# Optimization experiments

Measured on AMD Instinct MI355X. Metric: run time of the kernel, lower is better.

The kernel has to match this reference:

```python
import jax, jax.numpy as jnp
import numpy as np
import math

EMBED_DIM = 768
NUM_HEADS = 12
HEAD_DIM = EMBED_DIM // NUM_HEADS
R = 16
LORA_ALPHA = 16
SCALING = LORA_ALPHA / math.sqrt(R)  # 4.0
U = 1.0  # ramp_up_steps=0 -> u()=1.0


def lora_linear(x, W, b, A):
    # base F.linear + SingLoRA delta: delta_W = A @ A.T (symmetric)
    base = x @ W.T + b
    delta_W = A @ A.T  # [D, D]
    return base + (x @ delta_W.T) * (U * SCALING)


def setup_inputs() -> dict:
    key = jax.random.key(0)
    ks = jax.random.split(key, 16)
    B, S, D = 2, 2048, EMBED_DIM
    inv = 1.0 / math.sqrt(D)
    d = {
        'query': jax.random.normal(ks[0], (B, S, D), jnp.float32),
        'key': jax.random.normal(ks[1], (B, S, D), jnp.float32),
        'value': jax.random.normal(ks[2], (B, S, D), jnp.float32),
        'Wq': jax.random.normal(ks[3], (D, D), jnp.float32) * inv,
        'bq': jax.random.normal(ks[4], (D,), jnp.float32) * 0.01,
        'Aq': jax.random.normal(ks[5], (D, R), jnp.float32) * 0.01,
        'Wk': jax.random.normal(ks[6], (D, D), jnp.float32) * inv,
        'bk': jax.random.normal(ks[7], (D,), jnp.float32) * 0.01,
        'Ak': jax.random.normal(ks[8], (D, R), jnp.float32) * 0.01,
        'Wv': jax.random.normal(ks[9], (D, D), jnp.float32) * inv,
        'bv': jax.random.normal(ks[10], (D,), jnp.float32) * 0.01,
        'Av': jax.random.normal(ks[11], (D, R), jnp.float32) * 0.01,
        'Wo': jax.random.normal(ks[12], (D, D), jnp.float32) * inv,
        'bo': jax.random.normal(ks[13], (D,), jnp.float32) * 0.01,
    }
    return d


def reference(query, key, value, Wq, bq, Aq, Wk, bk, Ak, Wv, bv, Av, Wo, bo):
    B, S, D = query.shape
    H, hd = NUM_HEADS, HEAD_DIM
    q = lora_linear(query, Wq, bq, Aq)
    k = lora_linear(key, Wk, bk, Ak)
    v = lora_linear(value, Wv, bv, Av)
    # [B, S, D] -> [B, H, S, hd]
    q = q.reshape(B, S, H, hd).transpose(0, 2, 1, 3)
    k = k.reshape(B, S, H, hd).transpose(0, 2, 1, 3)
    v = v.reshape(B, S, H, hd).transpose(0, 2, 1, 3)
    scores = jnp.einsum('bhqd,bhkd->bhqk', q, k) / math.sqrt(hd)
    attn = jax.nn.softmax(scores, axis=-1)
    out = jnp.einsum('bhqk,bhkd->bhqd', attn, v)  # [B, H, S, hd]
    out = out.transpose(0, 2, 1, 3).reshape(B, S, D)
    out = out @ Wo.T + bo
    return out
```

## Files before the change

kernel.cpp:

```cpp
#include <hip/hip_runtime.h>
#include <math.h>
#include <stdint.h>

#define D 768
#define S 2048
#define B_ 2
#define NROWS 4096
#define H 12
#define HD 64
#define R_ 16

typedef _Float16 half_t;
typedef _Float16 half8 __attribute__((ext_vector_type(8)));
typedef _Float16 half4 __attribute__((ext_vector_type(4)));
typedef float floatx4 __attribute__((ext_vector_type(4)));

#define MFMA32(a, b, c) __builtin_amdgcn_mfma_f32_16x16x32_f16(a, b, c, 0, 0, 0)
#define MFMA16(a, b, c) __builtin_amdgcn_mfma_f32_16x16x16f16(a, b, c, 0, 0, 0)
#define EXP2F(x) __builtin_amdgcn_exp2f(x)

__device__ __forceinline__ void gl_lds16(const void* gp, half_t* lp) {
  __builtin_amdgcn_global_load_lds(
      (const __attribute__((address_space(1))) void*)(gp),
      (__attribute__((address_space(3))) void*)(lp), 16, 0, 0);
}

__global__ __launch_bounds__(256) void prep_kernel(
    const float* __restrict__ q, const float* __restrict__ k,
    const float* __restrict__ v, half_t* __restrict__ xq,
    half_t* __restrict__ xk, half_t* __restrict__ xv,
    const float* __restrict__ Wq, const float* __restrict__ Aq,
    const float* __restrict__ Wk, const float* __restrict__ Ak,
    const float* __restrict__ Wv, const float* __restrict__ Av,
    const float* __restrict__ Wo, half_t* __restrict__ Mq,
    half_t* __restrict__ Mk, half_t* __restrict__ Mv,
    half_t* __restrict__ Mo) {
  const int bid = blockIdx.x;
  if (bid < 9216) {
    const int y = bid / 3072;
    const float* x = (y == 0) ? q : (y == 1) ? k : v;
    half_t* o = (y == 0) ? xq : (y == 1) ? xk : xv;
    int i = (bid - y * 3072) * 1024 + threadIdx.x * 4;
    float4 vv = *reinterpret_cast<const float4*>(x + i);
    half_t tmp[4] = {(half_t)vv.x, (half_t)vv.y, (half_t)vv.z, (half_t)vv.w};
    *reinterpret_cast<uint64_t*>(o + i) = *reinterpret_cast<uint64_t*>(tmp);
  } else {
    const int u = bid - 9216;
    const int y = u / 2304;
    const float* W = (y == 0) ? Wq : (y == 1) ? Wk : (y == 2) ? Wv : Wo;
    const float* A = (y == 0) ? Aq : (y == 1) ? Ak : (y == 2) ? Av : nullptr;
    half_t* M = (y == 0) ? Mq : (y == 1) ? Mk : (y == 2) ? Mv : Mo;
    int idx = (u - y * 2304) * 256 + threadIdx.x;
    int j = idx / D;
    int kk = idx - j * D;
    float acc = W[idx];
    if (A != nullptr) {
      float s = 0.f;
#pragma unroll
      for (int r = 0; r < R_; ++r) s += A[kk * R_ + r] * A[j * R_ + r];
      acc += 4.0f * s;
    }
    M[idx] = (half_t)acc;
  }
}

__global__ __launch_bounds__(256) void gemm_qkv_kernel(
    const half_t* __restrict__ x0, const half_t* __restrict__ x1,
    const half_t* __restrict__ x2, const half_t* __restrict__ m0,
    const half_t* __restrict__ m1, const half_t* __restrict__ m2,
    const float* __restrict__ b0, const float* __restrict__ b1,
    const float* __restrict__ b2, half_t* __restrict__ o0,
    half_t* __restrict__ o1, half_t* __restrict__ o2) {
  constexpr int AG = 8;
  constexpr int G = AG + 16;
  constexpr int PB = G * 512;
  constexpr int TRS = 72;
  __shared__ __align__(16) half_t smem[2 * PB];

  const int z = blockIdx.z;
  const half_t* X = (z == 0) ? x0 : (z == 1) ? x1 : x2;
  const half_t* M = (z == 0) ? m0 : (z == 1) ? m1 : m2;
  const float* bias = (z == 0) ? b0 : (z == 1) ? b1 : b2;
  half_t* Out = (z == 0) ? o0 : (z == 1) ? o1 : o2;

  const int tid = threadIdx.x;
  const int lane = tid & 63;
  const int wv = tid >> 6;
  const int lr = lane & 15;
  const int lq = lane >> 4;
  const int row0 = blockIdx.y * 64;
  const int j0 = blockIdx.x * 128;
  const int wc = wv;

  floatx4 acc[4][2] = {};

#define GSTAGE(bufi, k0)                                                       \
  do {                                                                         \
    _Pragma("unroll") for (int gi = 0; gi < 6; ++gi) {                         \
      int g = wv * 6 + gi;                                                     \
      if (g < AG) {                                                            \
        int t = g >> 1, c = g & 1;                                             \
        gl_lds16(                                                              \
            X + (size_t)(row0 + t * 16 + lr) * D + (k0) + c * 32 + lq * 8,     \
            smem + (bufi)*PB + g * 512);                                       \
      } else {                                                                 \
        int g2 = g - AG;                                                       \
        int u = g2 >> 1, c = g2 & 1;                                           \
        gl_lds16(                                                              \
            M + (size_t)(j0 + u * 16 + lr) * D + (k0) + c * 32 + lq * 8,       \
            smem + (bufi)*PB + AG * 512 + g2 * 512);                           \
      }                                                                        \
    }                                                                          \
  } while (0)

  GSTAGE(0, 0);
  __syncthreads();

  for (int it = 0; it < D / 64; ++it) {
    const int cur = it & 1;
    if (it + 1 < D / 64) GSTAGE(cur ^ 1, (it + 1) * 64);
    const half_t* Ab = smem + cur * PB;
    const half_t* Bb = Ab + AG * 512;
#pragma unroll
    for (int c = 0; c < 2; ++c) {
      half8 af[4], bf[2];
#pragma unroll
      for (int t = 0; t < 4; ++t)
        af[t] = *reinterpret_cast<const half8*>(
            &Ab[((t * 2 + c) * 64 + lane) * 8]);
#pragma unroll
      for (int u = 0; u < 2; ++u)
        bf[u] = *reinterpret_cast<const half8*>(
            &Bb[(((wc * 2 + u) * 2 + c) * 64 + lane) * 8]);
#pragma unroll
      for (int t = 0; t < 4; ++t)
#pragma unroll
        for (int u = 0; u < 2; ++u) acc[t][u] = MFMA32(af[t], bf[u], acc[t][u]);
    }
    __syncthreads();
  }
#undef GSTAGE

  float bv[2];
#pragma unroll
  for (int u = 0; u < 2; ++u) bv[u] = bias[j0 + (wc * 2 + u) * 16 + lr];

  if (z == 2) {
#pragma unroll
    for (int t = 0; t < 4; ++t) {
#pragma unroll
      for (int u = 0; u < 2; ++u) {
        int c_local = (wc * 2 + u) * 16 + lr;
#pragma unroll
        for (int r = 0; r < 4; ++r) {
          int r_local = t * 16 + lq * 4 + r;
          smem[c_local * TRS + r_local] = (half_t)(acc[t][u][r] + bv[u]);
        }
      }
    }
    __syncthreads();
    const int bb = row0 >> 11;
    const int s_base = row0 & 2047;
#pragma unroll
    for (int it = 0; it < 4; ++it) {
      int unit = it * 256 + tid;
      int c_local = unit >> 3;
      int chunk = unit & 7;
      half8 vv =
          *reinterpret_cast<const half8*>(&smem[c_local * TRS + chunk * 8]);
      int gc = j0 + c_local;
      int hh = gc >> 6, dd = gc & 63;
      *reinterpret_cast<half8*>(
          &Out[((size_t)(bb * H + hh) * HD + dd) * S + s_base + chunk * 8]) = vv;
    }
    return;
  }

#pragma unroll
  for (int t = 0; t < 4; ++t) {
#pragma unroll
    for (int u = 0; u < 2; ++u) {
#pragma unroll
      for (int r = 0; r < 4; ++r) {
        int gr = row0 + t * 16 + lq * 4 + r;
        int gc = j0 + (wc * 2 + u) * 16 + lr;
        Out[(size_t)gr * D + gc] = (half_t)(acc[t][u][r] + bv[u]);
      }
    }
  }
}

__global__ __launch_bounds__(256) void gemm_o_kernel(
    const half_t* __restrict__ Xh, const half_t* __restrict__ M,
    const float* __restrict__ bias, float* __restrict__ Out) {
  constexpr int AG = 8;
  constexpr int G = AG + 16;
  constexpr int PB = G * 512;
  __shared__ __align__(16) half_t smem[2 * PB];

  const int tid = threadIdx.x;
  const int lane = tid & 63;
  const int wv = tid >> 6;
  const int lr = lane & 15;
  const int lq = lane >> 4;
  const int row0 = blockIdx.y * 64;
  const int j0 = blockIdx.x * 128;
  const int wc = wv;

  floatx4 acc[4][2] = {};

#define GSTAGE(bufi, k0)                                                       \
  do {                                                                         \
    _Pragma("unroll") for (int gi = 0; gi < 6; ++gi) {                         \
      int g = wv * 6 + gi;                                                     \
      if (g < AG) {                                                            \
        int t = g >> 1, c = g & 1;                                             \
        gl_lds16(                                                              \
            Xh + (size_t)(row0 + t * 16 + lr) * D + (k0) + c * 32 + lq * 8,    \
            smem + (bufi)*PB + g * 512);                                       \
      } else {                                                                 \
        int g2 = g - AG;                                                       \
        int u = g2 >> 1, c = g2 & 1;                                           \
        gl_lds16(                                                              \
            M + (size_t)(j0 + u * 16 + lr) * D + (k0) + c * 32 + lq * 8,       \
            smem + (bufi)*PB + AG * 512 + g2 * 512);                           \
      }                                                                        \
    }                                                                          \
  } while (0)

  GSTAGE(0, 0);
  __syncthreads();

  for (int it = 0; it < D / 64; ++it) {
    const int cur = it & 1;
    if (it + 1 < D / 64) GSTAGE(cur ^ 1, (it + 1) * 64);
    const half_t* Ab = smem + cur * PB;
    const half_t* Bb = Ab + AG * 512;
#pragma unroll
    for (int c = 0; c < 2; ++c) {
      half8 af[4], bf[2];
#pragma unroll
      for (int t = 0; t < 4; ++t)
        af[t] = *reinterpret_cast<const half8*>(
            &Ab[((t * 2 + c) * 64 + lane) * 8]);
#pragma unroll
      for (int u = 0; u < 2; ++u)
        bf[u] = *reinterpret_cast<const half8*>(
            &Bb[(((wc * 2 + u) * 2 + c) * 64 + lane) * 8]);
#pragma unroll
      for (int t = 0; t < 4; ++t)
#pragma unroll
        for (int u = 0; u < 2; ++u) acc[t][u] = MFMA32(af[t], bf[u], acc[t][u]);
    }
    __syncthreads();
  }
#undef GSTAGE

  float bv[2];
#pragma unroll
  for (int u = 0; u < 2; ++u) bv[u] = bias[j0 + (wc * 2 + u) * 16 + lr];
#pragma unroll
  for (int t = 0; t < 4; ++t) {
#pragma unroll
    for (int u = 0; u < 2; ++u) {
#pragma unroll
      for (int r = 0; r < 4; ++r) {
        int gr = row0 + t * 16 + lq * 4 + r;
        int gc = j0 + (wc * 2 + u) * 16 + lr;
        Out[(size_t)gr * D + gc] = acc[t][u][r] + bv[u];
      }
    }
  }
}

__global__ __launch_bounds__(512, 6) void attn_mfma_kernel(
    const half_t* __restrict__ Qh, const half_t* __restrict__ Kh,
    const half_t* __restrict__ Vt_g, half_t* __restrict__ Oh) {
  __shared__ __align__(16) half_t smem[16384];
  half_t* Ks = smem;
  half_t* Vs = smem + 8192;

  const int tid = threadIdx.x;
  const int lane = tid & 63;
  const int wv = tid >> 6;
  const int t_ = wv & 3;
  const int half_ = wv >> 2;
  const int lr = lane & 15;
  const int lq = lane >> 4;
  const int q0 = blockIdx.x * 64;
  const int h = blockIdx.y;
  const int b = blockIdx.z;
  const size_t base = (size_t)b * S * D + h * HD;
  const size_t vtbase = (size_t)(b * H + h) * HD * (size_t)S;
  const int qw = q0 + t_ * 16;

  const half_t qscale = (half_t)0.18033688f;
  half8 qf[2];
#pragma unroll
  for (int c = 0; c < 2; ++c) {
    half8 qv = *reinterpret_cast<const half8*>(
        &Qh[base + (size_t)(qw + lr) * D + c * 32 + lq * 8]);
#pragma unroll
    for (int j = 0; j < 8; ++j) qv[j] = qv[j] * qscale;
    qf[c] = qv;
  }

  half4 ones;
#pragma unroll
  for (int j = 0; j < 4; ++j) ones[j] = (half_t)1.0f;

  floatx4 o[4] = {};
  floatx4 ol = {};

#define STAGE(bufi, kb)                                                        \
  do {                                                                         \
    _Pragma("unroll") for (int gi = 0; gi < 2; ++gi) {                         \
      int g = wv * 2 + gi;                                                     \
      if (g < 8) {                                                             \
        int u = g >> 1, c = g & 1;                                             \
        gl_lds16(                                                              \
            Kh + base + (size_t)((kb) + u * 16 + lr) * D + c * 32 + lq * 8,    \
            Ks + (bufi)*4096 + g * 512);                                       \
      } else {                                                                 \
        int gv = g - 8;                                                        \
        int ud = gv >> 1, c = gv & 1;                                          \
        gl_lds16(                                                              \
            Vt_g + vtbase + (size_t)(ud * 16 + lr) * S + (kb) + c * 32 +       \
                lq * 8,                                                        \
            Vs + (bufi)*4096 + gv * 512);                                      \
      }                                                                        \
    }                                                                          \
  } while (0)

  STAGE(0, 0);
  __syncthreads();

  for (int it = 0; it < S / 64; ++it) {
    const int cur = it & 1;
    if (it + 1 < S / 64) STAGE(cur ^ 1, (it + 1) * 64);

#pragma unroll
    for (int ui = 0; ui < 2; ++ui) {
      const int u = half_ * 2 + ui;
      half8 kf0 = *reinterpret_cast<const half8*>(
          &Ks[cur * 4096 + ((u * 2 + 0) * 64 + lane) * 8]);
      half8 kf1 = *reinterpret_cast<const half8*>(
          &Ks[cur * 4096 + ((u * 2 + 1) * 64 + lane) * 8]);
      floatx4 st = {};
      st = MFMA32(kf0, qf[0], st);
      st = MFMA32(kf1, qf[1], st);
      half4 pf;
      pf[0] = (half_t)EXP2F(st[0]);
      pf[1] = (half_t)EXP2F(st[1]);
      pf[2] = (half_t)EXP2F(st[2]);
      pf[3] = (half_t)EXP2F(st[3]);
#pragma unroll
      for (int ud = 0; ud < 4; ++ud) {
        half4 vf = *reinterpret_cast<const half4*>(
            &Vs[cur * 4096 + ((ud * 2 + (u >> 1)) * 64 +
                              ((((u & 1) * 2) + (lq >> 1)) * 16 + lr)) *
                                 8 +
                (lq & 1) * 4]);
        o[ud] = MFMA16(pf, vf, o[ud]);
      }
      ol = MFMA16(pf, ones, ol);
    }
    __syncthreads();
  }
#undef STAGE

  float* red = (float*)smem;
  const int slot = t_ * 64 + lane;
  if (half_ == 1) {
#pragma unroll
    for (int comp = 0; comp < 16; ++comp)
      red[comp * 260 + slot] = o[comp >> 2][comp & 3];
#pragma unroll
    for (int r = 0; r < 4; ++r) red[(16 + r) * 260 + slot] = ol[r];
  }
  __syncthreads();
  if (half_ == 0) {
#pragma unroll
    for (int comp = 0; comp < 16; ++comp)
      o[comp >> 2][comp & 3] += red[comp * 260 + slot];
    float linv[4];
#pragma unroll
    for (int r = 0; r < 4; ++r)
      linv[r] = 1.0f / (ol[r] + red[(16 + r) * 260 + slot]);
#pragma unroll
    for (int ud = 0; ud < 4; ++ud) {
#pragma unroll
      for (int r = 0; r < 4; ++r) {
        int row = qw + lq * 4 + r;
        int col = h * HD + ud * 16 + lr;
        Oh[(size_t)(b * S + row) * D + col] = (half_t)(o[ud][r] * linv[r]);
      }
    }
  }
}

extern "C" void kernel_launch(void* const* d_in, const int* in_sizes, int n_in,
                              void* d_out, int out_size, void* d_ws,
                              size_t ws_size, hipStream_t stream) {
  const float* query = (const float*)d_in[0];
  const float* key   = (const float*)d_in[1];
  const float* value = (const float*)d_in[2];
  const float* Wq = (const float*)d_in[3];
  const float* bq = (const float*)d_in[4];
  const float* Aq = (const float*)d_in[5];
  const float* Wk = (const float*)d_in[6];
  const float* bk = (const float*)d_in[7];
  const float* Ak = (const float*)d_in[8];
  const float* Wv = (const float*)d_in[9];
  const float* bv = (const float*)d_in[10];
  const float* Av = (const float*)d_in[11];
  const float* Wo = (const float*)d_in[12];
  const float* bo = (const float*)d_in[13];
  float* out = (float*)d_out;

  half_t* hw = (half_t*)d_ws;
  const size_t XSZ = (size_t)NROWS * D;
  const size_t MSZ = (size_t)D * D;
  half_t* xq = hw;
  half_t* xk = xq + XSZ;
  half_t* xv = xk + XSZ;
  half_t* qh = xv + XSZ;
  half_t* kh = qh + XSZ;
  half_t* vt = kh + XSZ;
  half_t* ab = vt + XSZ;
  half_t* Mq = ab + XSZ;
  half_t* Mk = Mq + MSZ;
  half_t* Mv = Mk + MSZ;
  half_t* Mo = Mv + MSZ;

  prep_kernel<<<18432, 256, 0, stream>>>(query, key, value, xq, xk, xv, Wq, Aq,
                                         Wk, Ak, Wv, Av, Wo, Mq, Mk, Mv, Mo);

  dim3 gq(D / 128, NROWS / 64, 3);
  gemm_qkv_kernel<<<gq, 256, 0, stream>>>(xq, xk, xv, Mq, Mk, Mv, bq, bk, bv,
                                          qh, kh, vt);

  dim3 ga(S / 64, H, B_);
  attn_mfma_kernel<<<ga, 512, 0, stream>>>(qh, kh, vt, ab);

  dim3 go(D / 128, NROWS / 64, 1);
  gemm_o_kernel<<<go, 256, 0, stream>>>(ab, Mo, bo, out);
}
```

Baseline: 233.0 us.

## Load per-wave B/K operands directly into registers and halve O-projection tile width

Result: slower. 349.6 us (+50.0%).

```diff
diff --git a/kernel.cpp b/kernel.cpp
--- a/kernel.cpp
+++ b/kernel.cpp
@@ -71,11 +71,8 @@
     const float* __restrict__ b0, const float* __restrict__ b1,
     const float* __restrict__ b2, half_t* __restrict__ o0,
     half_t* __restrict__ o1, half_t* __restrict__ o2) {
-  constexpr int AG = 8;
-  constexpr int G = AG + 16;
-  constexpr int PB = G * 512;
   constexpr int TRS = 72;
-  __shared__ __align__(16) half_t smem[2 * PB];
+  __shared__ __align__(16) half_t smem[9216];
 
   const int z = blockIdx.z;
   const half_t* X = (z == 0) ? x0 : (z == 1) ? x1 : x2;
@@ -93,53 +90,60 @@
   const int wc = wv;
 
   floatx4 acc[4][2] = {};
-
-#define GSTAGE(bufi, k0)                                                       \
-  do {                                                                         \
-    _Pragma("unroll") for (int gi = 0; gi < 6; ++gi) {                         \
-      int g = wv * 6 + gi;                                                     \
-      if (g < AG) {                                                            \
-        int t = g >> 1, c = g & 1;                                             \
-        gl_lds16(                                                              \
-            X + (size_t)(row0 + t * 16 + lr) * D + (k0) + c * 32 + lq * 8,     \
-            smem + (bufi)*PB + g * 512);                                       \
-      } else {                                                                 \
-        int g2 = g - AG;                                                       \
-        int u = g2 >> 1, c = g2 & 1;                                           \
-        gl_lds16(                                                              \
-            M + (size_t)(j0 + u * 16 + lr) * D + (k0) + c * 32 + lq * 8,       \
-            smem + (bufi)*PB + AG * 512 + g2 * 512);                           \
-      }                                                                        \
+  half8 bA[2][2], bB[2][2];
+
+#define STAGEA(bufi, k0)                                                       \
+  do {                                                                         \
+    _Pragma("unroll") for (int gi = 0; gi < 2; ++gi) {                         \
+      int g = wv * 2 + gi;                                                     \
+      int t = g >> 1, c = g & 1;                                               \
+      gl_lds16(X + (size_t)(row0 + t * 16 + lr) * D + (k0) + c * 32 + lq * 8,  \
+               smem + (bufi)*4096 + g * 512);                                  \
     }                                                                          \
   } while (0)
 
-  GSTAGE(0, 0);
+#define LOADB(BF, k0)                                                          \
+  do {                                                                         \
+    _Pragma("unroll") for (int u = 0; u < 2; ++u)                              \
+        _Pragma("unroll") for (int c = 0; c < 2; ++c) BF[u][c] =               \
+        *reinterpret_cast<const half8*>(                                       \
+            &M[(size_t)(j0 + (wc * 2 + u) * 16 + lr) * D + (k0) + c * 32 +     \
+               lq * 8]);                                                       \
+  } while (0)
+
+#define COMPUTEG(BF, bufi)                                                     \
+  do {                                                                         \
+    _Pragma("unroll") for (int c = 0; c < 2; ++c) {                            \
+      half8 af[4];                                                             \
+      _Pragma("unroll") for (int t = 0; t < 4; ++t) af[t] =                    \
+          *reinterpret_cast<const half8*>(                                     \
+              &smem[(bufi)*4096 + ((t * 2 + c) * 64 + lane) * 8]);             \
+      _Pragma("unroll") for (int t = 0; t < 4; ++t)                            \
+          _Pragma("unroll") for (int u = 0; u < 2; ++u) acc[t][u] =            \
+          MFMA32(af[t], BF[u][c], acc[t][u]);                                  \
+    }                                                                          \
+  } while (0)
+
+  STAGEA(0, 0);
+  LOADB(bA, 0);
   __syncthreads();
 
-  for (int it = 0; it < D / 64; ++it) {
-    const int cur = it & 1;
-    if (it + 1 < D / 64) GSTAGE(cur ^ 1, (it + 1) * 64);
-    const half_t* Ab = smem + cur * PB;
-    const half_t* Bb = Ab + AG * 512;
-#pragma unroll
-    for (int c = 0; c < 2; ++c) {
-      half8 af[4], bf[2];
-#pragma unroll
-      for (int t = 0; t < 4; ++t)
-        af[t] = *reinterpret_cast<const half8*>(
-            &Ab[((t * 2 + c) * 64 + lane) * 8]);
-#pragma unroll
-      for (int u = 0; u < 2; ++u)
-        bf[u] = *reinterpret_cast<const half8*>(
-            &Bb[(((wc * 2 + u) * 2 + c) * 64 + lane) * 8]);
-#pragma unroll
-      for (int t = 0; t < 4; ++t)
-#pragma unroll
-        for (int u = 0; u < 2; ++u) acc[t][u] = MFMA32(af[t], bf[u], acc[t][u]);
-    }
-    __syncthreads();
-  }
-#undef GSTAGE
+#pragma unroll 1
+  for (int it = 0; it < D / 64; it += 2) {
+    STAGEA(1, (it + 1) * 64);
+    LOADB(bB, (it + 1) * 64);
+    COMPUTEG(bA, 0);
+    __syncthreads();
+    if (it + 2 < D / 64) {
+      STAGEA(0, (it + 2) * 64);
+      LOADB(bA, (it + 2) * 64);
+    }
+    COMPUTEG(bB, 1);
+    __syncthreads();
+  }
+#undef STAGEA
+#undef LOADB
+#undef COMPUTEG
 
   float bv[2];
 #pragma unroll
@@ -193,10 +197,7 @@
 __global__ __launch_bounds__(256) void gemm_o_kernel(
     const half_t* __restrict__ Xh, const half_t* __restrict__ M,
     const float* __restrict__ bias, float* __restrict__ Out) {
-  constexpr int AG = 8;
-  constexpr int G = AG + 16;
-  constexpr int PB = G * 512;
-  __shared__ __align__(16) half_t smem[2 * PB];
+  __shared__ __align__(16) half_t smem[8192];
 
   const int tid = threadIdx.x;
   const int lane = tid & 63;
@@ -204,71 +205,70 @@
   const int lr = lane & 15;
   const int lq = lane >> 4;
   const int row0 = blockIdx.y * 64;
-  const int j0 = blockIdx.x * 128;
+  const int j0 = blockIdx.x * 64;
   const int wc = wv;
 
-  floatx4 acc[4][2] = {};
-
-#define GSTAGE(bufi, k0)                                                       \
-  do {                                                                         \
-    _Pragma("unroll") for (int gi = 0; gi < 6; ++gi) {                         \
-      int g = wv * 6 + gi;                                                     \
-      if (g < AG) {                                                            \
-        int t = g >> 1, c = g & 1;                                             \
-        gl_lds16(                                                              \
-            Xh + (size_t)(row0 + t * 16 + lr) * D + (k0) + c * 32 + lq * 8,    \
-            smem + (bufi)*PB + g * 512);                                       \
-      } else {                                                                 \
-        int g2 = g - AG;                                                       \
-        int u = g2 >> 1, c = g2 & 1;                                           \
-        gl_lds16(                                                              \
-            M + (size_t)(j0 + u * 16 + lr) * D + (k0) + c * 32 + lq * 8,       \
-            smem + (bufi)*PB + AG * 512 + g2 * 512);                           \
-      }                                                                        \
+  floatx4 acc[4] = {};
+  half8 bA[2], bB[2];
+
+#define STAGEA(bufi, k0)                                                       \
+  do {                                                                         \
+    _Pragma("unroll") for (int gi = 0; gi < 2; ++gi) {                         \
+      int g = wv * 2 + gi;                                                     \
+      int t = g >> 1, c = g & 1;                                               \
+      gl_lds16(Xh + (size_t)(row0 + t * 16 + lr) * D + (k0) + c * 32 + lq * 8, \
+               smem + (bufi)*4096 + g * 512);                                  \
     }                                                                          \
   } while (0)
 
-  GSTAGE(0, 0);
+#define LOADB(BF, k0)                                                          \
+  do {                                                                         \
+    _Pragma("unroll") for (int c = 0; c < 2; ++c) BF[c] =                      \
+        *reinterpret_cast<const half8*>(                                       \
+            &M[(size_t)(j0 + wc * 16 + lr) * D + (k0) + c * 32 + lq * 8]);     \
+  } while (0)
+
+#define COMPUTEG(BF, bufi)                                                     \
+  do {                                                                         \
+    _Pragma("unroll") for (int c = 0; c < 2; ++c) {                            \
+      half8 af[4];                                                             \
+      _Pragma("unroll") for (int t = 0; t < 4; ++t) af[t] =                    \
+          *reinterpret_cast<const half8*>(                                     \
+              &smem[(bufi)*4096 + ((t * 2 + c) * 64 + lane) * 8]);             \
+      _Pragma("unroll") for (int t = 0; t < 4; ++t) acc[t] =                   \
+          MFMA32(af[t], BF[c], acc[t]);                                        \
+    }                                                                          \
+  } while (0)
+
+  STAGEA(0, 0);
+  LOADB(bA, 0);
   __syncthreads();
 
-  for (int it = 0; it < D / 64; ++it) {
-    const int cur = it & 1;
-    if (it + 1 < D / 64) GSTAGE(cur ^ 1, (it + 1) * 64);
-    const half_t* Ab = smem + cur * PB;
-    const half_t* Bb = Ab + AG * 512;
-#pragma unroll
-    for (int c = 0; c < 2; ++c) {
-      half8 af[4], bf[2];
-#pragma unroll
-      for (int t = 0; t < 4; ++t)
-        af[t] = *reinterpret_cast<const half8*>(
-            &Ab[((t * 2 + c) * 64 + lane) * 8]);
-#pragma unroll
-      for (int u = 0; u < 2; ++u)
-        bf[u] = *reinterpret_cast<const half8*>(
-            &Bb[(((wc * 2 + u) * 2 + c) * 64 + lane) * 8]);
-#pragma unroll
-      for (int t = 0; t < 4; ++t)
-#pragma unroll
-        for (int u = 0; u < 2; ++u) acc[t][u] = MFMA32(af[t], bf[u], acc[t][u]);
-    }
-    __syncthreads();
-  }
-#undef GSTAGE
-
-  float bv[2];
-#pragma unroll
-  for (int u = 0; u < 2; ++u) bv[u] = bias[j0 + (wc * 2 + u) * 16 + lr];
+#pragma unroll 1
+  for (int it = 0; it < D / 64; it += 2) {
+    STAGEA(1, (it + 1) * 64);
+    LOADB(bB, (it + 1) * 64);
+    COMPUTEG(bA, 0);
+    __syncthreads();
+    if (it + 2 < D / 64) {
+      STAGEA(0, (it + 2) * 64);
+      LOADB(bA, (it + 2) * 64);
+    }
+    COMPUTEG(bB, 1);
+    __syncthreads();
+  }
+#undef STAGEA
+#undef LOADB
+#undef COMPUTEG
+
+  float bv = bias[j0 + wc * 16 + lr];
 #pragma unroll
   for (int t = 0; t < 4; ++t) {
 #pragma unroll
-    for (int u = 0; u < 2; ++u) {
-#pragma unroll
-      for (int r = 0; r < 4; ++r) {
-        int gr = row0 + t * 16 + lq * 4 + r;
-        int gc = j0 + (wc * 2 + u) * 16 + lr;
-        Out[(size_t)gr * D + gc] = acc[t][u][r] + bv[u];
-      }
+    for (int r = 0; r < 4; ++r) {
+      int gr = row0 + t * 16 + lq * 4 + r;
+      int gc = j0 + wc * 16 + lr;
+      Out[(size_t)gr * D + gc] = acc[t][r] + bv;
     }
   }
 }
@@ -276,9 +276,8 @@
 __global__ __launch_bounds__(512, 6) void attn_mfma_kernel(
     const half_t* __restrict__ Qh, const half_t* __restrict__ Kh,
     const half_t* __restrict__ Vt_g, half_t* __restrict__ Oh) {
-  __shared__ __align__(16) half_t smem[16384];
-  half_t* Ks = smem;
-  half_t* Vs = smem + 8192;
+  __shared__ __align__(16) half_t smem[12288];
+  half_t* Vs = smem;
 
   const int tid = threadIdx.x;
   const int lane = tid & 63;
@@ -311,63 +310,70 @@
 
   floatx4 o[4] = {};
   floatx4 ol = {};
-
-#define STAGE(bufi, kb)                                                        \
-  do {                                                                         \
-    _Pragma("unroll") for (int gi = 0; gi < 2; ++gi) {                         \
-      int g = wv * 2 + gi;                                                     \
-      if (g < 8) {                                                             \
-        int u = g >> 1, c = g & 1;                                             \
-        gl_lds16(                                                              \
-            Kh + base + (size_t)((kb) + u * 16 + lr) * D + c * 32 + lq * 8,    \
-            Ks + (bufi)*4096 + g * 512);                                       \
-      } else {                                                                 \
-        int gv = g - 8;                                                        \
-        int ud = gv >> 1, c = gv & 1;                                          \
-        gl_lds16(                                                              \
-            Vt_g + vtbase + (size_t)(ud * 16 + lr) * S + (kb) + c * 32 +       \
-                lq * 8,                                                        \
-            Vs + (bufi)*4096 + gv * 512);                                      \
+  half8 kf0[2][2], kf1[2][2];
+
+#define STAGEV(bufi, kb)                                                       \
+  do {                                                                         \
+    int ud = wv >> 1, c = wv & 1;                                              \
+    gl_lds16(                                                                  \
+        Vt_g + vtbase + (size_t)(ud * 16 + lr) * S + (kb) + c * 32 + lq * 8,   \
+        Vs + (bufi)*4096 + wv * 512);                                          \
+  } while (0)
+
+#define LOADK(KF, kb)                                                          \
+  do {                                                                         \
+    _Pragma("unroll") for (int ui = 0; ui < 2; ++ui)                           \
+        _Pragma("unroll") for (int c = 0; c < 2; ++c) KF[ui][c] =              \
+        *reinterpret_cast<const half8*>(                                       \
+            &Kh[base + (size_t)((kb) + (half_ * 2 + ui) * 16 + lr) * D +       \
+                c * 32 + lq * 8]);                                             \
+  } while (0)
+
+#define ACOMPUTE(KF, CUR)                                                      \
+  do {                                                                         \
+    _Pragma("unroll") for (int ui = 0; ui < 2; ++ui) {                         \
+      const int u = half_ * 2 + ui;                                            \
+      floatx4 st = {};                                                         \
+      st = MFMA32(KF[ui][0], qf[0], st);                                       \
+      st = MFMA32(KF[ui][1], qf[1], st);                                       \
+      half4 pf;                                                                \
+      pf[0] = (half_t)EXP2F(st[0]);                                            \
+      pf[1] = (half_t)EXP2F(st[1]);                                            \
+      pf[2] = (half_t)EXP2F(st[2]);                                            \
+      pf[3] = (half_t)EXP2F(st[3]);                                            \
+      _Pragma("unroll") for (int ud = 0; ud < 4; ++ud) {                       \
+        half4 vf = *reinterpret_cast<const half4*>(                            \
+            &Vs[(CUR)*4096 +                                                   \
+                ((ud * 2 + (u >> 1)) * 64 +                                    \
+                 ((((u & 1) * 2) + (lq >> 1)) * 16 + lr)) *                    \
+                    8 +                                                        \
+                (lq & 1) * 4]);                                                \
+        o[ud] = MFMA16(pf, vf, o[ud]);                                         \
       }                                                                        \
+      ol = MFMA16(pf, ones, ol);                                               \
     }                                                                          \
   } while (0)
 
-  STAGE(0, 0);
+  STAGEV(0, 0);
+  LOADK(kf0, 0);
   __syncthreads();
 
-  for (int it = 0; it < S / 64; ++it) {
-    const int cur = it & 1;
-    if (it + 1 < S / 64) STAGE(cur ^ 1, (it + 1) * 64);
-
-#pragma unroll
-    for (int ui = 0; ui < 2; ++ui) {
-      const int u = half_ * 2 + ui;
-      half8 kf0 = *reinterpret_cast<const half8*>(
-          &Ks[cur * 4096 + ((u * 2 + 0) * 64 + lane) * 8]);
-      half8 kf1 = *reinterpret_cast<const half8*>(
-          &Ks[cur * 4096 + ((u * 2 + 1) * 64 + lane) * 8]);
-      floatx4 st = {};
-      st = MFMA32(kf0, qf[0], st);
-      st = MFMA32(kf1, qf[1], st);
-      half4 pf;
-      pf[0] = (half_t)EXP2F(st[0]);
-      pf[1] = (half_t)EXP2F(st[1]);
-      pf[2] = (half_t)EXP2F(st[2]);
-      pf[3] = (half_t)EXP2F(st[3]);
-#pragma unroll
-      for (int ud = 0; ud < 4; ++ud) {
-        half4 vf = *reinterpret_cast<const half4*>(
-            &Vs[cur * 4096 + ((ud * 2 + (u >> 1)) * 64 +
-                              ((((u & 1) * 2) + (lq >> 1)) * 16 + lr)) *
-                                 8 +
-                (lq & 1) * 4]);
-        o[ud] = MFMA16(pf, vf, o[ud]);
-      }
-      ol = MFMA16(pf, ones, ol);
-    }
-    __syncthreads();
-  }
-#undef STAGE
+#pragma unroll 1
+  for (int it = 0; it < S / 64; it += 2) {
+    STAGEV(1, (it + 1) * 64);
+    LOADK(kf1, (it + 1) * 64);
+    ACOMPUTE(kf0, 0);
+    __syncthreads();
+    if (it + 2 < S / 64) {
+      STAGEV(0, (it + 2) * 64);
+      LOADK(kf0, (it + 2) * 64);
+    }
+    ACOMPUTE(kf1, 1);
+    __syncthreads();
+  }
+#undef STAGEV
+#undef LOADK
+#undef ACOMPUTE
 
   float* red = (float*)smem;
   const int slot = t_ * 64 + lane;
@@ -443,6 +449,6 @@
   dim3 ga(S / 64, H, B_);
   attn_mfma_kernel<<<ga, 512, 0, stream>>>(qh, kh, vt, ab);
 
-  dim3 go(D / 128, NROWS / 64, 1);
+  dim3 go(D / 64, NROWS / 64, 1);
   gemm_o_kernel<<<go, 256, 0, stream>>>(ab, Mo, bo, out);
 }
```

## Write V in MFMA-fragment layout and shrink output-projection GEMM tiles

Applied to the files above, without the earlier changes.

After: 223.1 us. -4.3%, faster.

```diff
diff --git a/kernel.cpp b/kernel.cpp
--- a/kernel.cpp
+++ b/kernel.cpp
@@ -24,6 +24,7 @@
       (const __attribute__((address_space(1))) void*)(gp),
       (__attribute__((address_space(3))) void*)(lp), 16, 0, 0);
 }
+
 
 __global__ __launch_bounds__(256) void prep_kernel(
     const float* __restrict__ q, const float* __restrict__ k,
@@ -74,7 +75,6 @@
   constexpr int AG = 8;
   constexpr int G = AG + 16;
   constexpr int PB = G * 512;
-  constexpr int TRS = 72;
   __shared__ __align__(16) half_t smem[2 * PB];
 
   const int z = blockIdx.z;
@@ -146,32 +146,22 @@
   for (int u = 0; u < 2; ++u) bv[u] = bias[j0 + (wc * 2 + u) * 16 + lr];
 
   if (z == 2) {
+    const int bb = row0 >> 11;
+    const int kb = (row0 & 2047) >> 6;
 #pragma unroll
     for (int t = 0; t < 4; ++t) {
 #pragma unroll
       for (int u = 0; u < 2; ++u) {
-        int c_local = (wc * 2 + u) * 16 + lr;
-#pragma unroll
-        for (int r = 0; r < 4; ++r) {
-          int r_local = t * 16 + lq * 4 + r;
-          smem[c_local * TRS + r_local] = (half_t)(acc[t][u][r] + bv[u]);
-        }
+        int gc = j0 + (wc * 2 + u) * 16 + lr;
+        int hh = gc >> 6;
+        int ud = (wc * 2 + u) & 3;
+        half4 hv;
+#pragma unroll
+        for (int r = 0; r < 4; ++r) hv[r] = (half_t)(acc[t][u][r] + bv[u]);
+        size_t addr = ((size_t)(bb * H + hh) * HD) * S + (size_t)kb * 4096 +
+                      (ud * 2 + (t >> 1)) * 512 + lane * 8 + (t & 1) * 4;
+        *reinterpret_cast<half4*>(&Out[addr]) = hv;
       }
-    }
-    __syncthreads();
-    const int bb = row0 >> 11;
-    const int s_base = row0 & 2047;
-#pragma unroll
-    for (int it = 0; it < 4; ++it) {
-      int unit = it * 256 + tid;
-      int c_local = unit >> 3;
-      int chunk = unit & 7;
-      half8 vv =
-          *reinterpret_cast<const half8*>(&smem[c_local * TRS + chunk * 8]);
-      int gc = j0 + c_local;
-      int hh = gc >> 6, dd = gc & 63;
-      *reinterpret_cast<half8*>(
-          &Out[((size_t)(bb * H + hh) * HD + dd) * S + s_base + chunk * 8]) = vv;
     }
     return;
   }
@@ -194,7 +184,7 @@
     const half_t* __restrict__ Xh, const half_t* __restrict__ M,
     const float* __restrict__ bias, float* __restrict__ Out) {
   constexpr int AG = 8;
-  constexpr int G = AG + 16;
+  constexpr int G = 16;
   constexpr int PB = G * 512;
   __shared__ __align__(16) half_t smem[2 * PB];
 
@@ -204,15 +194,16 @@
   const int lr = lane & 15;
   const int lq = lane >> 4;
   const int row0 = blockIdx.y * 64;
-  const int j0 = blockIdx.x * 128;
-  const int wc = wv;
-
-  floatx4 acc[4][2] = {};
+  const int j0 = blockIdx.x * 64;
+  const int wr = wv >> 1;
+  const int wc = wv & 1;
+
+  floatx4 acc[2][2] = {};
 
 #define GSTAGE(bufi, k0)                                                       \
   do {                                                                         \
-    _Pragma("unroll") for (int gi = 0; gi < 6; ++gi) {                         \
-      int g = wv * 6 + gi;                                                     \
+    _Pragma("unroll") for (int gi = 0; gi < 4; ++gi) {                         \
+      int g = wv * 4 + gi;                                                     \
       if (g < AG) {                                                            \
         int t = g >> 1, c = g & 1;                                             \
         gl_lds16(                                                              \
@@ -238,17 +229,17 @@
     const half_t* Bb = Ab + AG * 512;
 #pragma unroll
     for (int c = 0; c < 2; ++c) {
-      half8 af[4], bf[2];
-#pragma unroll
-      for (int t = 0; t < 4; ++t)
+      half8 af[2], bf[2];
+#pragma unroll
+      for (int t = 0; t < 2; ++t)
         af[t] = *reinterpret_cast<const half8*>(
-            &Ab[((t * 2 + c) * 64 + lane) * 8]);
+            &Ab[(((wr * 2 + t) * 2 + c) * 64 + lane) * 8]);
 #pragma unroll
       for (int u = 0; u < 2; ++u)
         bf[u] = *reinterpret_cast<const half8*>(
             &Bb[(((wc * 2 + u) * 2 + c) * 64 + lane) * 8]);
 #pragma unroll
-      for (int t = 0; t < 4; ++t)
+      for (int t = 0; t < 2; ++t)
 #pragma unroll
         for (int u = 0; u < 2; ++u) acc[t][u] = MFMA32(af[t], bf[u], acc[t][u]);
     }
@@ -260,12 +251,12 @@
 #pragma unroll
   for (int u = 0; u < 2; ++u) bv[u] = bias[j0 + (wc * 2 + u) * 16 + lr];
 #pragma unroll
-  for (int t = 0; t < 4; ++t) {
+  for (int t = 0; t < 2; ++t) {
 #pragma unroll
     for (int u = 0; u < 2; ++u) {
 #pragma unroll
       for (int r = 0; r < 4; ++r) {
-        int gr = row0 + t * 16 + lq * 4 + r;
+        int gr = row0 + (wr * 2 + t) * 16 + lq * 4 + r;
         int gc = j0 + (wc * 2 + u) * 16 + lr;
         Out[(size_t)gr * D + gc] = acc[t][u][r] + bv[u];
       }
@@ -275,7 +266,7 @@
 
 __global__ __launch_bounds__(512, 6) void attn_mfma_kernel(
     const half_t* __restrict__ Qh, const half_t* __restrict__ Kh,
-    const half_t* __restrict__ Vt_g, half_t* __restrict__ Oh) {
+    const half_t* __restrict__ Vt2, half_t* __restrict__ Oh) {
   __shared__ __align__(16) half_t smem[16384];
   half_t* Ks = smem;
   half_t* Vs = smem + 8192;
@@ -323,11 +314,8 @@
             Ks + (bufi)*4096 + g * 512);                                       \
       } else {                                                                 \
         int gv = g - 8;                                                        \
-        int ud = gv >> 1, c = gv & 1;                                          \
-        gl_lds16(                                                              \
-            Vt_g + vtbase + (size_t)(ud * 16 + lr) * S + (kb) + c * 32 +       \
-                lq * 8,                                                        \
-            Vs + (bufi)*4096 + gv * 512);                                      \
+        gl_lds16(Vt2 + vtbase + (size_t)(kb)*64 + gv * 512 + lane * 8,         \
+                 Vs + (bufi)*4096 + gv * 512);                                 \
       }                                                                        \
     }                                                                          \
   } while (0)
@@ -339,6 +327,7 @@
     const int cur = it & 1;
     if (it + 1 < S / 64) STAGE(cur ^ 1, (it + 1) * 64);
 
+    half4 pf[2];
 #pragma unroll
     for (int ui = 0; ui < 2; ++ui) {
       const int u = half_ * 2 + ui;
@@ -349,22 +338,26 @@
       floatx4 st = {};
       st = MFMA32(kf0, qf[0], st);
       st = MFMA32(kf1, qf[1], st);
-      half4 pf;
-      pf[0] = (half_t)EXP2F(st[0]);
-      pf[1] = (half_t)EXP2F(st[1]);
-      pf[2] = (half_t)EXP2F(st[2]);
-      pf[3] = (half_t)EXP2F(st[3]);
-#pragma unroll
-      for (int ud = 0; ud < 4; ++ud) {
-        half4 vf = *reinterpret_cast<const half4*>(
-            &Vs[cur * 4096 + ((ud * 2 + (u >> 1)) * 64 +
-                              ((((u & 1) * 2) + (lq >> 1)) * 16 + lr)) *
-                                 8 +
-                (lq & 1) * 4]);
-        o[ud] = MFMA16(pf, vf, o[ud]);
+      pf[ui][0] = (half_t)EXP2F(st[0]);
+      pf[ui][1] = (half_t)EXP2F(st[1]);
+      pf[ui][2] = (half_t)EXP2F(st[2]);
+      pf[ui][3] = (half_t)EXP2F(st[3]);
+    }
+#pragma unroll
+    for (int ud = 0; ud < 4; ++ud) {
+      half8 vf8 = *reinterpret_cast<const half8*>(
+          &Vs[cur * 4096 + ((ud * 2 + half_) * 64 + lane) * 8]);
+      half4 vlo, vhi;
+#pragma unroll
+      for (int j = 0; j < 4; ++j) {
+        vlo[j] = vf8[j];
+        vhi[j] = vf8[4 + j];
       }
-      ol = MFMA16(pf, ones, ol);
-    }
+      o[ud] = MFMA16(pf[0], vlo, o[ud]);
+      o[ud] = MFMA16(pf[1], vhi, o[ud]);
+    }
+    ol = MFMA16(pf[0], ones, ol);
+    ol = MFMA16(pf[1], ones, ol);
     __syncthreads();
   }
 #undef STAGE
@@ -443,6 +436,6 @@
   dim3 ga(S / 64, H, B_);
   attn_mfma_kernel<<<ga, 512, 0, stream>>>(qh, kh, vt, ab);
 
-  dim3 go(D / 128, NROWS / 64, 1);
+  dim3 go(D / 64, NROWS / 64, 1);
   gemm_o_kernel<<<go, 256, 0, stream>>>(ab, Mo, bo, out);
 }
```
